# Optimization experiments

Hardware: AMD Instinct MI355X
Metric: run time of the kernel (lower is better)

The kernel has to match this reference:

```python
import jax, jax.numpy as jnp
import numpy as np

N = 10000; E = 320000; NFEAT = 500; NHID = 256; C = 16; K = 64
GAMMA = 4; ALPHA = 0.1; BETA = 1.0; EPS = 0.1; LAMDA = 0.5; W1 = 0.5

def _init(key, shape, scale=0.05):
    return jax.random.normal(key, shape, dtype=jnp.float32) * scale

def setup_inputs():
    key = jax.random.key(0)
    ks = jax.random.split(key, 24)
    return {
        "x": jax.random.normal(ks[0], (N, NFEAT), dtype=jnp.float32),
        "edge_index": jax.random.randint(ks[1], (2, E), 0, N),
        "edge_weight": jax.random.uniform(ks[2], (E,), dtype=jnp.float32),
        "adj_weight": jax.random.uniform(ks[3], (E,), dtype=jnp.float32),
        "connect": jax.random.uniform(ks[4], (N, N), dtype=jnp.float32),
        "confidence_in": jax.random.uniform(ks[5], (2, E), dtype=jnp.float32),
        "lin1_w": _init(ks[6], (NHID, NFEAT)),
        "lin1_b": jnp.zeros((NHID,), jnp.float32),
        "lin2_w": _init(ks[7], (C, NHID)),
        "lin2_b": jnp.zeros((C,), jnp.float32),
        "lin_a_w": _init(ks[8], (NHID, N), 0.01),
        "lin_a_b": jnp.zeros((NHID,), jnp.float32),
        "lin_n_w": _init(ks[9], (C, C)),
        "lin_n_b": jnp.zeros((C,), jnp.float32),
        "left_w": _init(ks[10], (C, C)),
        "att_w": _init(ks[11], (1, C)),
        "v_w": _init(ks[12], (K, NHID)),
        "v_b": jnp.zeros((K,), jnp.float32),
        "W": _init(ks[13], (C, C)),
        "conf_param": jnp.zeros((3,), jnp.float32),
        "b_param": jnp.zeros((1,), jnp.float32),
    }

def _forward(x, edge_index, edge_weight, adj_weight, connect, confidence_in,
             lin1_w, lin1_b, lin2_w, lin2_b, lin_a_w, lin_a_b, lin_n_w, lin_n_b,
             left_w, att_w, v_w, v_b, W, conf_param, b_param):
    row, col = edge_index[0], edge_index[1]

    def spmm(vals, out_idx, M):
        # COO sparse @ dense: scatter-add per-edge vals * gathered rows of M
        return jax.ops.segment_sum(vals[:, None] * M, out_idx, num_segments=N)

    x_a = connect @ lin_a_w.T + lin_a_b            # [N, NHID]
    h = x @ lin1_w.T + lin1_b
    h = jax.nn.relu((1.0 - LAMDA) * h + LAMDA * x_a)
    raw = h                                        # [N, NHID]
    h = h @ lin2_w.T + lin2_b                      # [N, C]

    # neighbor label distribution: row-normalized adj @ one_hot(argmax softmax)
    y_hat = jnp.argmax(jax.nn.softmax(h, axis=1), axis=1)
    one_hot = jax.nn.one_hot(y_hat, C, dtype=h.dtype)
    nei = spmm(adj_weight, row, one_hot[col])
    s = nei.sum(axis=1, keepdims=True)
    nei = jnp.where(s != 0, nei / jnp.where(s == 0, 1.0, s), 0.0)

    x_n = jax.nn.relu(nei @ lin_n_w.T + lin_n_b)
    h = (1.0 - W1) * h + W1 * x_n
    init = h

    # per-edge attention-based confidence mixed with input confidences
    lx = h @ left_w.T
    confi = jax.nn.relu(lx[row] + lx[col])
    confi = jax.nn.sigmoid((confi @ att_w.T)[:, 0])
    w = jax.nn.softmax(conf_param)
    conf = confi * w[0] + confidence_in[0] * w[1] + confidence_in[1] * w[2]  # [E]

    V = raw @ v_w.T + v_b                          # [N, K]
    U = spmm(adj_weight, row, V[col]) @ jnp.linalg.inv(V.T @ V)
    eyeK = jnp.eye(K, dtype=h.dtype)

    def edge_mask_score(score):
        S = score ** 2
        ss = jnp.sort(S)
        q1, q3 = ss[E // 4], ss[3 * E // 4]
        thr = (q3 + 1.5 * (q3 - q1)) * conf        # [E]
        mask = (S < thr).astype(h.dtype)
        return (score + b_param[0]) * mask

    def update_u(U, V):
        SS = edge_mask_score(edge_weight - jnp.sum(U[row] * V[col], axis=1))
        temp = spmm(SS, row, V[col]) + U @ (V.T @ V) + EPS * (h @ (h.T @ V))
        inver = jnp.linalg.inv((1.0 + EPS) * (V.T @ V) + BETA * eyeK)
        return temp @ inver

    def update_v(U, V):
        SS = edge_mask_score(edge_weight - jnp.sum(V[row] * U[col], axis=1))
        # A^T @ U: scatter over col with U[row]
        temp = spmm(SS, col, U[row]) + V @ (U.T @ U) + EPS * (h @ (h.T @ U))
        inver = jnp.linalg.inv((1.0 + EPS) * (U.T @ U) + BETA * eyeK)
        return temp @ inver

    for j in range(GAMMA):
        if j % 2 == 0:
            U = update_u(U, V)
        else:
            V = update_v(U, V)

    prop = U @ (h.T @ V).T                         # [N, C]
    out = (1.0 - ALPHA) * prop + ALPHA * init
    return out @ W

def reference(x, edge_index, edge_weight, adj_weight, connect, confidence_in,
              lin1_w, lin1_b, lin2_w, lin2_b, lin_a_w, lin_a_b, lin_n_w, lin_n_b,
              left_w, att_w, v_w, v_b, W, conf_param, b_param):
    return _forward(x, edge_index, edge_weight, adj_weight, connect, confidence_in,
                    lin1_w, lin1_b, lin2_w, lin2_b, lin_a_w, lin_a_b, lin_n_w, lin_n_b,
                    left_w, att_w, v_w, v_b, W, conf_param, b_param)
```

## Files before the change

kernel.cpp:

```cpp
#include <hip/hip_runtime.h>
#include <cstddef>
#include <cstdint>


constexpr int kN  = 10000;
constexpr int kE  = 320000;
constexpr int kNH = 256;
constexpr int kC  = 16;
constexpr int kK  = 64;

struct SelState {
  int bin1[2]; int rem1[2];
  float thr_base;
};

typedef short bf16x8 __attribute__((ext_vector_type(8)));
typedef float f32x4 __attribute__((ext_vector_type(4)));
typedef ushort ushort8 __attribute__((ext_vector_type(8)));

__device__ __forceinline__ ushort f2bf(float x) {
  unsigned u = __float_as_uint(x);
  unsigned r = (u + 0x7fffu + ((u >> 16) & 1u)) >> 16;
  return (ushort)r;
}
__device__ __forceinline__ float bf2f(ushort h) {
  return __uint_as_float((unsigned)h << 16);
}
__device__ __forceinline__ int swz(int row, int byteInRow) {
  int chunk = (byteInRow >> 4) ^ ((row >> 1) & 3);
  return row * 64 + (chunk << 4) + (byteInRow & 15);
}

__global__ void split_bf(const float* __restrict__ B, ushort* __restrict__ hi,
                         ushort* __restrict__ lo, int N2, int K, int Kp)
{
  int t = blockIdx.x * 256 + threadIdx.x;
  if (t >= N2 * Kp) return;
  int r = t / Kp, c = t % Kp;
  float v = (c < K) ? B[(size_t)r * K + c] : 0.f;
  ushort h = f2bf(v);
  hi[t] = h;
  lo[t] = f2bf(v - bf2f(h));
}

template<int BN, bool ALO>
__global__ __launch_bounds__(256) void gemm_v3(
    const float* __restrict__ A, const ushort* __restrict__ Bhg,
    const ushort* __restrict__ Blg, const float* __restrict__ bias,
    float* __restrict__ out, int M, int K, int Kp, int KR, int outStride)
{
  __shared__ __align__(16) char sAh[64 * 64];
  __shared__ __align__(16) char sAl[ALO ? 64 * 64 : 16];
  __shared__ __align__(16) char sBh[BN * 64];
  __shared__ __align__(16) char sBl[BN * 64];
  const int t = threadIdx.x;
  const int lane = t & 63, w = t >> 6;
  const int bm = blockIdx.x * 64;
  const int k0 = blockIdx.z * KR;
  const int kend = min(K, k0 + KR);
  out += (size_t)blockIdx.z * M * outStride;
  constexpr int WN = BN / 64;
  constexpr int RB = WN;
  const int wc = (w % WN) * 64;
  const int wr = (w / WN) * (RB * 16);
  const int l15 = lane & 15;
  const int lByte = (lane >> 4) * 16;
  const int ar = t >> 2, ac = t & 3;

  f32x4 acc[RB][4] = {};
  for (int kt = k0; kt < kend; kt += 32) {
    {
      int gr = bm + ar, gk = kt + ac * 8;
      float v[8];
      if (gr < M && gk + 8 <= kend) {
        float4 v0 = *reinterpret_cast<const float4*>(A + (size_t)gr * K + gk);
        float4 v1 = *reinterpret_cast<const float4*>(A + (size_t)gr * K + gk + 4);
        v[0] = v0.x; v[1] = v0.y; v[2] = v0.z; v[3] = v0.w;
        v[4] = v1.x; v[5] = v1.y; v[6] = v1.z; v[7] = v1.w;
      } else {
#pragma unroll
        for (int q = 0; q < 8; q++)
          v[q] = (gr < M && gk + q < kend) ? A[(size_t)gr * K + gk + q] : 0.f;
      }
      ushort8 h8, l8;
#pragma unroll
      for (int q = 0; q < 8; q++) {
        ushort h = f2bf(v[q]); h8[q] = h;
        if (ALO) l8[q] = f2bf(v[q] - bf2f(h));
      }
      *reinterpret_cast<ushort8*>(sAh + swz(ar, ac * 16)) = h8;
      if (ALO) *reinterpret_cast<ushort8*>(sAl + swz(ar, ac * 16)) = l8;
    }
#pragma unroll
    for (int i2 = 0; i2 < BN / 64; i2++) {
      int idx = t + i2 * 256;
      int r = idx >> 2, c = idx & 3;
      size_t gb = (size_t)r * Kp + kt + c * 8;
      ushort8 hv = *reinterpret_cast<const ushort8*>(Bhg + gb);
      ushort8 lv = *reinterpret_cast<const ushort8*>(Blg + gb);
      *reinterpret_cast<ushort8*>(sBh + swz(r, c * 16)) = hv;
      *reinterpret_cast<ushort8*>(sBl + swz(r, c * 16)) = lv;
    }
    __syncthreads();
    bf16x8 bh[4], bl[4];
#pragma unroll
    for (int nb = 0; nb < 4; nb++) {
      int rr = wc + nb * 16 + l15;
      bh[nb] = *reinterpret_cast<const bf16x8*>(sBh + swz(rr, lByte));
      bl[nb] = *reinterpret_cast<const bf16x8*>(sBl + swz(rr, lByte));
    }
#pragma unroll
    for (int rb = 0; rb < RB; rb++) {
      int rr = wr + rb * 16 + l15;
      bf16x8 ah = *reinterpret_cast<const bf16x8*>(sAh + swz(rr, lByte));
#pragma unroll
      for (int nb = 0; nb < 4; nb++) {
        acc[rb][nb] = __builtin_amdgcn_mfma_f32_16x16x32_bf16(ah, bh[nb], acc[rb][nb], 0, 0, 0);
        acc[rb][nb] = __builtin_amdgcn_mfma_f32_16x16x32_bf16(ah, bl[nb], acc[rb][nb], 0, 0, 0);
      }
      if (ALO) {
        bf16x8 al = *reinterpret_cast<const bf16x8*>(sAl + swz(rr, lByte));
#pragma unroll
        for (int nb = 0; nb < 4; nb++)
          acc[rb][nb] = __builtin_amdgcn_mfma_f32_16x16x32_bf16(al, bh[nb], acc[rb][nb], 0, 0, 0);
      }
    }
    __syncthreads();
  }
#pragma unroll
  for (int rb = 0; rb < RB; rb++) {
#pragma unroll
    for (int nb = 0; nb < 4; nb++) {
      int colg = wc + nb * 16 + l15;
      float bv = bias ? bias[colg] : 0.f;
#pragma unroll
      for (int j = 0; j < 4; j++) {
        int rowg = bm + wr + rb * 16 + (lane >> 4) * 4 + j;
        if (rowg < M) out[(size_t)rowg * outStride + colg] = acc[rb][nb][j] + bv;
      }
    }
  }
}

__global__ void reduce_raw(const float4* __restrict__ Pa, const float4* px,
                           const float* __restrict__ ba, const float* __restrict__ b1,
                           float4* rawOut)
{
  int t = blockIdx.x * 256 + threadIdx.x;
  if (t >= kN * kNH / 4) return;
  const int sl = kN * kNH / 4;
  float4 s = Pa[t];
#pragma unroll
  for (int p = 1; p < 5; p++) {
    float4 q = Pa[t + (size_t)p * sl];
    s.x += q.x; s.y += q.y; s.z += q.z; s.w += q.w;
  }
  float4 pxv = px[t];
  int c4 = t & 63;
  float4 vba = reinterpret_cast<const float4*>(ba)[c4];
  float4 vb1 = reinterpret_cast<const float4*>(b1)[c4];
  float4 r;
  r.x = fmaxf(0.5f * (s.x + vba.x) + 0.5f * (pxv.x + vb1.x), 0.f);
  r.y = fmaxf(0.5f * (s.y + vba.y) + 0.5f * (pxv.y + vb1.y), 0.f);
  r.z = fmaxf(0.5f * (s.z + vba.z) + 0.5f * (pxv.z + vb1.z), 0.f);
  r.w = fmaxf(0.5f * (s.w + vba.w) + 0.5f * (pxv.w + vb1.w), 0.f);
  rawOut[t] = r;
}

__global__ void gemm_rowdot(const float* __restrict__ A, const float* __restrict__ Bw,
                            const float* __restrict__ bias, float* __restrict__ outm,
                            int M, int N2, int K2)
{
  int t = blockIdx.x * 256 + threadIdx.x;
  if (t >= M * N2) return;
  int i = t / N2, j = t % N2;
  const float4* a = reinterpret_cast<const float4*>(A + (size_t)i * K2);
  const float4* b = reinterpret_cast<const float4*>(Bw + (size_t)j * K2);
  float s = bias ? bias[j] : 0.f;
  int q4 = K2 >> 2;
  for (int q = 0; q < q4; q++) {
    float4 av = a[q], bv = b[q];
    s += av.x * bv.x + av.y * bv.y + av.z * bv.z + av.w * bv.w;
  }
  outm[t] = s;
}

__global__ void argmax16(const float* __restrict__ h, int* __restrict__ y, int n)
{
  int i = blockIdx.x * 256 + threadIdx.x;
  if (i >= n) return;
  const float* r = h + (size_t)i * 16;
  float m = r[0]; int a = 0;
#pragma unroll
  for (int j = 1; j < 16; j++) { float v = r[j]; if (v > m) { m = v; a = j; } }
  y[i] = a;
}

__global__ void scatter_nei(const int* __restrict__ row, const int* __restrict__ col,
                            const float* __restrict__ aw, const int* __restrict__ yhat,
                            float* nei, int E)
{
  int e = blockIdx.x * 256 + threadIdx.x;
  if (e >= E) return;
  atomicAdd(&nei[(size_t)row[e] * 16 + yhat[col[e]]], aw[e]);
}

__global__ void norm_xn_h(const float* __restrict__ nei, const float* __restrict__ h16,
                          const float* __restrict__ lnw, const float* __restrict__ lnb,
                          float* __restrict__ hc, int n)
{
  int i = blockIdx.x * 256 + threadIdx.x;
  if (i >= n) return;
  float nv[16]; float s = 0.f;
#pragma unroll
  for (int c = 0; c < 16; c++) { nv[c] = nei[(size_t)i * 16 + c]; s += nv[c]; }
  float inv = (s != 0.f) ? 1.f / s : 0.f;
#pragma unroll
  for (int j = 0; j < 16; j++) {
    float xn = lnb[j];
#pragma unroll
    for (int c = 0; c < 16; c++) xn += (nv[c] * inv) * lnw[j * 16 + c];
    xn = fmaxf(xn, 0.f);
    hc[(size_t)i * 16 + j] = 0.5f * h16[(size_t)i * 16 + j] + 0.5f * xn;
  }
}

__global__ void edge_conf(const int* __restrict__ row, const int* __restrict__ col,
                          const float* __restrict__ lx, const float* __restrict__ attw,
                          const float* __restrict__ ci, const float* __restrict__ cp,
                          float* __restrict__ conf, int E)
{
  int e = blockIdx.x * 256 + threadIdx.x;
  if (e >= E) return;
  float p0 = cp[0], p1 = cp[1], p2 = cp[2];
  float m = fmaxf(p0, fmaxf(p1, p2));
  float e0 = expf(p0 - m), e1 = expf(p1 - m), e2 = expf(p2 - m);
  float inv = 1.f / (e0 + e1 + e2);
  float w0 = e0 * inv, w1 = e1 * inv, w2 = e2 * inv;
  const float* a = lx + (size_t)row[e] * 16;
  const float* b = lx + (size_t)col[e] * 16;
  float s = 0.f;
#pragma unroll
  for (int c = 0; c < 16; c++) s += fmaxf(a[c] + b[c], 0.f) * attw[c];
  float cf = 1.f / (1.f + expf(-s));
  conf[e] = cf * w0 + ci[e] * w1 + ci[(size_t)E + e] * w2;
}

__global__ void csr_count(const int* __restrict__ row, const int* __restrict__ col,
                          int* cntR, int* cntC, int E)
{
  int e = blockIdx.x * 256 + threadIdx.x;
  if (e >= E) return;
  atomicAdd(&cntR[row[e]], 1);
  atomicAdd(&cntC[col[e]], 1);
}

__global__ __launch_bounds__(1024) void scan2(const int* __restrict__ cntR, const int* __restrict__ cntC,
                                              int* __restrict__ startR, int* __restrict__ startC, int n)
{
  __shared__ int part[1024];
  const int t = threadIdx.x;
  for (int pass = 0; pass < 2; ++pass) {
    const int* cnt = pass ? cntC : cntR;
    int* start = pass ? startC : startR;
    int base = t * 10;
    int loc[10]; int s = 0;
#pragma unroll
    for (int q = 0; q < 10; q++) { int idx = base + q; int v = (idx < n) ? cnt[idx] : 0; loc[q] = v; s += v; }
    part[t] = s;
    __syncthreads();
    for (int off = 1; off < 1024; off <<= 1) {
      int v = part[t];
      int u = (t >= off) ? part[t - off] : 0;
      __syncthreads();
      part[t] = v + u;
      __syncthreads();
    }
    int run = part[t] - s;
#pragma unroll
    for (int q = 0; q < 10; q++) { int idx = base + q; if (idx < n) start[idx] = run; run += loc[q]; }
    if (t == 1023) start[n] = part[1023];
    __syncthreads();
  }
}

__global__ void csr_fill(const int* __restrict__ row, const int* __restrict__ col,
                         const int* __restrict__ startR, const int* __restrict__ startC,
                         int* fillR, int* fillC, int* eR, int* eC,
                         int* othR, int* othC, int E)
{
  int e = blockIdx.x * 256 + threadIdx.x;
  if (e >= E) return;
  int r = row[e], c = col[e];
  int pr = startR[r] + atomicAdd(&fillR[r], 1);
  eR[pr] = e; othR[pr] = c;
  int pc = startC[c] + atomicAdd(&fillC[c], 1);
  eC[pc] = e; othC[pc] = r;
}

__global__ void spmm_gather(const float* __restrict__ vals, const int* __restrict__ start,
                            const int* __restrict__ eids, const int* __restrict__ oth,
                            const float* __restrict__ Msrc, float* __restrict__ T, int n)
{
  int wid = blockIdx.x * 4 + (threadIdx.x >> 6);
  int lane = threadIdx.x & 63;
  if (wid >= n) return;
  int p = start[wid], pend = start[wid + 1];
  float acc = 0.f;
  for (; p + 4 <= pend; p += 4) {
    int e0 = eids[p], e1 = eids[p + 1], e2 = eids[p + 2], e3 = eids[p + 3];
    int o0 = oth[p], o1 = oth[p + 1], o2 = oth[p + 2], o3 = oth[p + 3];
    float m0 = Msrc[(size_t)o0 * 64 + lane];
    float m1 = Msrc[(size_t)o1 * 64 + lane];
    float m2 = Msrc[(size_t)o2 * 64 + lane];
    float m3 = Msrc[(size_t)o3 * 64 + lane];
    acc += vals[e0] * m0 + vals[e1] * m1 + vals[e2] * m2 + vals[e3] * m3;
  }
  for (; p < pend; ++p)
    acc += vals[eids[p]] * Msrc[(size_t)oth[p] * 64 + lane];
  T[(size_t)wid * 64 + lane] = acc;
}

__global__ __launch_bounds__(256) void gram_partial(const float* __restrict__ A, const float* __restrict__ B,
                                                    float* __restrict__ P, int n, int Ka, int chunk)
{
  __shared__ float sA[8 * 64];
  __shared__ float sB[8 * 64];
  const int t = threadIdx.x;
  const int tpa = 256 / Ka;
  const int cpt = 64 / tpa;
  const int a  = t / tpa;
  const int c0 = (t % tpa) * cpt;
  float acc[16];
#pragma unroll
  for (int j = 0; j < 16; j++) acc[j] = 0.f;
  int r0 = blockIdx.x * chunk;
  int r1 = min(n, r0 + chunk);
  for (int rb = r0; rb < r1; rb += 8) {
    int nb = min(8, r1 - rb);
    for (int q = t; q < nb * Ka; q += 256) sA[(q / Ka) * 64 + (q % Ka)] = A[(size_t)(rb + q / Ka) * Ka + (q % Ka)];
    for (int q = t; q < nb * 64; q += 256) sB[q] = B[(size_t)rb * 64 + q];
    __syncthreads();
    for (int r = 0; r < nb; r++) {
      float av = sA[r * 64 + a];
      const float* sb = &sB[r * 64 + c0];
      if (cpt == 16) {
#pragma unroll
        for (int j = 0; j < 16; j++) acc[j] += av * sb[j];
      } else {
#pragma unroll
        for (int j = 0; j < 4; j++) acc[j] += av * sb[j];
      }
    }
    __syncthreads();
  }
  float* p = P + (size_t)blockIdx.x * Ka * 64 + a * 64 + c0;
  if (cpt == 16) {
#pragma unroll
    for (int j = 0; j < 16; j++) p[j] = acc[j];
  } else {
#pragma unroll
    for (int j = 0; j < 4; j++) p[j] = acc[j];
  }
}

__global__ void gram_reduce(const float* __restrict__ P, float* __restrict__ G, int cells, int parts)
{
  int c = blockIdx.x * 256 + threadIdx.x;
  if (c >= cells) return;
  float s = 0.f;
  for (int p = 0; p < parts; p++) s += P[(size_t)p * cells + c];
  G[c] = s;
}

__global__ __launch_bounds__(256) void inverse64_spd(
    const float* __restrict__ G, float* __restrict__ Gi, float alpha, float beta,
    const float* __restrict__ hTX, float* __restrict__ Gp, float* __restrict__ Hp)
{
  __shared__ __align__(16) float A[64 * 132];
  __shared__ __align__(16) float prow[128];
  __shared__ float fcol[64];
  const int t = threadIdx.x;
  for (int q = t; q < 64 * 128; q += 256) {
    int r = q >> 7, c = q & 127;
    float v;
    if (c < 64) v = alpha * G[r * 64 + c] + ((c == r) ? beta : 0.f);
    else        v = (c - 64 == r) ? 1.f : 0.f;
    A[r * 132 + c] = v;
  }
  __syncthreads();
  const int i  = t >> 2;
  const int c0 = (t & 3) * 32;
  for (int k = 0; k < 64; k++) {
    if (t < 128) prow[t] = A[k * 132 + t];
    else if (t < 192) fcol[t - 128] = A[(t - 128) * 132 + k];
    __syncthreads();
    float pinv = 1.f / prow[k];
    float f = fcol[i];
    float4* Ar = reinterpret_cast<float4*>(&A[i * 132 + c0]);
    const float4* pr = reinterpret_cast<const float4*>(&prow[c0]);
    if (i == k) {
#pragma unroll
      for (int j = 0; j < 8; j++) {
        float4 p = pr[j];
        p.x *= pinv; p.y *= pinv; p.z *= pinv; p.w *= pinv;
        Ar[j] = p;
      }
    } else {
#pragma unroll
      for (int j = 0; j < 8; j++) {
        float4 p = pr[j]; float4 av = Ar[j];
        av.x -= f * (p.x * pinv); av.y -= f * (p.y * pinv);
        av.z -= f * (p.z * pinv); av.w -= f * (p.w * pinv);
        Ar[j] = av;
      }
    }
    __syncthreads();
  }
  for (int q = t; q < 4096; q += 256) Gi[q] = A[(q >> 6) * 132 + 64 + (q & 63)];
  if (Gp) {
    for (int q = t; q < 4096; q += 256) {
      int r = q >> 6, k = q & 63;
      float s = 0.f;
#pragma unroll 8
      for (int j = 0; j < 64; j++) s += G[r * 64 + j] * A[j * 132 + 64 + k];
      Gp[q] = s;
    }
    for (int q = t; q < 1024; q += 256) {
      int c = q >> 6, k = q & 63;
      float s = 0.f;
#pragma unroll 8
      for (int j = 0; j < 64; j++) s += hTX[c * 64 + j] * A[j * 132 + 64 + k];
      Hp[q] = 0.1f * s;
    }
  }
}

__global__ void edge_score(const float* __restrict__ ew, const int* __restrict__ row,
                           const int* __restrict__ col, const float* __restrict__ Ma,
                           const float* __restrict__ Mb, float* __restrict__ score,
                           int* __restrict__ hist1, int* __restrict__ h2a,
                           int* __restrict__ h2b, int E)
{
  int e = blockIdx.x * 256 + threadIdx.x;
  if (e < 65536) { hist1[e] = 0; h2a[e] = 0; h2b[e] = 0; }
  if (e >= E) return;
  const float4* a = reinterpret_cast<const float4*>(Ma + (size_t)row[e] * 64);
  const float4* b = reinterpret_cast<const float4*>(Mb + (size_t)col[e] * 64);
  float s = 0.f;
#pragma unroll
  for (int q = 0; q < 16; q++) {
    float4 av = a[q], bv = b[q];
    s += av.x * bv.x + av.y * bv.y + av.z * bv.z + av.w * bv.w;
  }
  score[e] = ew[e] - s;
}

__global__ void hist_pass1(const float* __restrict__ score, int* __restrict__ h, int E)
{
  int e = blockIdx.x * 256 + threadIdx.x;
  if (e >= E) return;
  float sc = score[e];
  unsigned u = __float_as_uint(sc * sc);
  atomicAdd(&h[u >> 16], 1);
}

__global__ void hist_pass2(const float* __restrict__ score, const SelState* __restrict__ sel,
                           int* __restrict__ h2a, int* __restrict__ h2b, int E)
{
  int e = blockIdx.x * 256 + threadIdx.x;
  if (e >= E) return;
  float sc = score[e];
  unsigned u = __float_as_uint(sc * sc);
  int top = (int)(u >> 16);
  if (top == sel->bin1[0]) atomicAdd(&h2a[u & 0xFFFF], 1);
  if (top == sel->bin1[1]) atomicAdd(&h2b[u & 0xFFFF], 1);
}

__global__ __launch_bounds__(256) void select_scan(
    const int* __restrict__ h0, const int* __restrict__ h1,
    int stage, SelState* sel)
{
  const int t = threadIdx.x;
  __shared__ int part[256];
  __shared__ int foundBin[2];
  __shared__ float qsh[2];
  const int per = 65536 / 256;
  for (int tgt = 0; tgt < 2; tgt++) {
    const int* H = tgt ? h1 : h0;
    int R = (stage == 1) ? (tgt ? (3 * kE / 4) : (kE / 4)) : sel->rem1[tgt];
    int lsum = 0;
    for (int b = 0; b < per; b++) lsum += H[t * per + b];
    part[t] = lsum;
    __syncthreads();
    for (int off = 1; off < 256; off <<= 1) {
      int v = part[t];
      int u = (t >= off) ? part[t - off] : 0;
      __syncthreads();
      part[t] = v + u;
      __syncthreads();
    }
    int cum = part[t] - lsum;
    int fb = -1, fr = 0;
    for (int b = 0; b < per; b++) {
      int c = H[t * per + b];
      if (R >= cum && R < cum + c) { fb = t * per + b; fr = R - cum; }
      cum += c;
    }
    if (fb >= 0) {
      foundBin[tgt] = fb;
      if (stage == 1) { sel->bin1[tgt] = fb; sel->rem1[tgt] = fr; }
    }
    __syncthreads();
    if (stage == 2 && t == 0) {
      unsigned u = ((unsigned)sel->bin1[tgt] << 16) | (unsigned)foundBin[tgt];
      qsh[tgt] = __uint_as_float(u);
    }
    __syncthreads();
  }
  if (stage == 2 && t == 0) {
    float q1 = qsh[0], q3 = qsh[1];
    sel->thr_base = q3 + 1.5f * (q3 - q1);
  }
}

__global__ void mask_SS(const float* __restrict__ score, const float* __restrict__ conf,
                        const SelState* __restrict__ sel, const float* __restrict__ bp,
                        float* __restrict__ SS, int E)
{
  int e = blockIdx.x * 256 + threadIdx.x;
  if (e >= E) return;
  float sc = score[e];
  float thr = sel->thr_base * conf[e];
  SS[e] = (sc * sc < thr) ? (sc + bp[0]) : 0.f;
}

__global__ void out_fused(const float* __restrict__ T, const float* __restrict__ Gi,
                          const float* __restrict__ X, const float* __restrict__ Gp,
                          const float* __restrict__ hc, const float* __restrict__ Hp,
                          float* __restrict__ Out, int n)
{
  int t = blockIdx.x * 256 + threadIdx.x;
  if (t >= n * 64) return;
  int i = t >> 6, k = t & 63;
  const float* ti = T + (size_t)i * 64;
  float s = 0.f;
#pragma unroll 8
  for (int j = 0; j < 64; j++) s += ti[j] * Gi[j * 64 + k];
  if (X) {
    const float* xi = X + (size_t)i * 64;
    float s2 = 0.f;
#pragma unroll 8
    for (int j = 0; j < 64; j++) s2 += xi[j] * Gp[j * 64 + k];
    s += s2;
    float s3 = 0.f;
#pragma unroll
    for (int c = 0; c < 16; c++) s3 += hc[(size_t)i * 16 + c] * Hp[c * 64 + k];
    s += s3;
  }
  Out[t] = s;
}

__global__ __launch_bounds__(256) void final_out(
    const float* __restrict__ Um, const float* __restrict__ hTV,
    const float* __restrict__ hc, const float* __restrict__ Wm,
    float* __restrict__ out, int n)
{
  __shared__ float sh[1024];
  __shared__ float sW[256];
  for (int q = threadIdx.x; q < 1024; q += 256) sh[q] = hTV[q];
  sW[threadIdx.x] = Wm[threadIdx.x & 255];
  __syncthreads();
  int i = blockIdx.x * 256 + threadIdx.x;
  if (i >= n) return;
  const float* u = Um + (size_t)i * 64;
  float pre[16];
#pragma unroll
  for (int c = 0; c < 16; c++) {
    float s = 0.f;
#pragma unroll
    for (int k = 0; k < 64; k++) s += u[k] * sh[c * 64 + k];
    pre[c] = 0.9f * s + 0.1f * hc[(size_t)i * 16 + c];
  }
#pragma unroll
  for (int j = 0; j < 16; j++) {
    float o = 0.f;
#pragma unroll
    for (int c = 0; c < 16; c++) o += pre[c] * sW[c * 16 + j];
    out[(size_t)i * 16 + j] = o;
  }
}

extern "C" void kernel_launch(void* const* d_in, const int* in_sizes, int n_in,
                              void* d_out, int out_size, void* d_ws, size_t ws_size,
                              hipStream_t stream)
{
  const float* x       = (const float*)d_in[0];
  const int*   eidx    = (const int*)d_in[1];
  const float* ew      = (const float*)d_in[2];
  const float* aw      = (const float*)d_in[3];
  const float* connect = (const float*)d_in[4];
  const float* ci      = (const float*)d_in[5];
  const float* lin1_w  = (const float*)d_in[6];
  const float* lin1_b  = (const float*)d_in[7];
  const float* lin2_w  = (const float*)d_in[8];
  const float* lin2_b  = (const float*)d_in[9];
  const float* lin_a_w = (const float*)d_in[10];
  const float* lin_a_b = (const float*)d_in[11];
  const float* lin_n_w = (const float*)d_in[12];
  const float* lin_n_b = (const float*)d_in[13];
  const float* left_w  = (const float*)d_in[14];
  const float* att_w   = (const float*)d_in[15];
  const float* v_w     = (const float*)d_in[16];
  const float* v_b     = (const float*)d_in[17];
  const float* Wm      = (const float*)d_in[18];
  const float* conf_p  = (const float*)d_in[19];
  const float* b_param = (const float*)d_in[20];
  const int* row = eidx;
  const int* col = eidx + kE;
  float* out = (float*)d_out;

  char* base = (char*)d_ws;
  size_t off = 0;
  auto alloc = [&](size_t bytes) -> void* {
    void* p = base + off;
    off += bytes;
    off = (off + 255) & ~(size_t)255;
    return p;
  };
  float* raw   = (float*)alloc((size_t)kN * kNH * 4);
  float* h16   = (float*)alloc((size_t)kN * kC * 4);
  float* hC    = (float*)alloc((size_t)kN * kC * 4);
  float* nei   = (float*)alloc((size_t)kN * kC * 4);
  float* lx    = (float*)alloc((size_t)kN * kC * 4);
  int*   yhat  = (int*)alloc((size_t)kN * 4);
  float* conf  = (float*)alloc((size_t)kE * 4);
  float* Va    = (float*)alloc((size_t)kN * kK * 4);
  float* Vb    = (float*)alloc((size_t)kN * kK * 4);
  float* Ua    = (float*)alloc((size_t)kN * kK * 4);
  float* Ub    = (float*)alloc((size_t)kN * kK * 4);
  float* T     = (float*)alloc((size_t)kN * kK * 4);
  float* score = (float*)alloc((size_t)kE * 4);
  float* SS    = (float*)alloc((size_t)kE * 4);
  float* G     = (float*)alloc(64 * 64 * 4);
  float* Gi    = (float*)alloc(64 * 64 * 4);
  float* Gp    = (float*)alloc(64 * 64 * 4);
  float* hTX   = (float*)alloc(kC * kK * 4);
  float* Hp    = (float*)alloc(kC * kK * 4);
  int* hist1   = (int*)alloc(65536 * 4);
  int* h2a     = (int*)alloc(65536 * 4);
  int* h2b     = (int*)alloc(65536 * 4);
  SelState* sel = (SelState*)alloc(sizeof(SelState));
  int* cntR    = (int*)alloc((size_t)kN * 4);
  int* cntC    = (int*)alloc((size_t)kN * 4);
  int* fillR   = (int*)alloc((size_t)kN * 4);
  int* fillC   = (int*)alloc((size_t)kN * 4);
  int* startR  = (int*)alloc((size_t)(kN + 1) * 4);
  int* startC  = (int*)alloc((size_t)(kN + 1) * 4);
  int* eR      = (int*)alloc((size_t)kE * 4);
  int* eC      = (int*)alloc((size_t)kE * 4);
  int* othR    = (int*)alloc((size_t)kE * 4);
  int* othC    = (int*)alloc((size_t)kE * 4);
  float* P     = (float*)alloc((size_t)100 * 4096 * 4);
  const int KpC = 10016, KpX = 512, KpV = 256;
  ushort* BcH = (ushort*)alloc((size_t)256 * KpC * 2);
  ushort* BcL = (ushort*)alloc((size_t)256 * KpC * 2);
  ushort* BxH = (ushort*)alloc((size_t)256 * KpX * 2);
  ushort* BxL = (ushort*)alloc((size_t)256 * KpX * 2);
  ushort* BvH = (ushort*)alloc((size_t)64 * KpV * 2);
  ushort* BvL = (ushort*)alloc((size_t)64 * KpV * 2);
  float* Pbig  = (float*)alloc((size_t)5 * kN * kNH * 4);

  const int eg  = (kE + 255) / 256;
  const int nkg = (kN * kK + 255) / 256;
  const int gwg = (kN + 3) / 4;

  split_bf<<<(256 * KpC + 255) / 256, 256, 0, stream>>>(lin_a_w, BcH, BcL, 256, 10000, KpC);
  split_bf<<<(256 * KpX + 255) / 256, 256, 0, stream>>>(lin1_w, BxH, BxL, 256, 500, KpX);
  split_bf<<<(64 * KpV + 255) / 256, 256, 0, stream>>>(v_w, BvH, BvL, 64, 256, KpV);

  {
    size_t csrSpan = (size_t)((char*)(fillC + kN) - (char*)cntR);
    (void)hipMemsetAsync(cntR, 0, csrSpan, stream);
  }
  csr_count<<<eg, 256, 0, stream>>>(row, col, cntR, cntC, kE);
  scan2<<<1, 1024, 0, stream>>>(cntR, cntC, startR, startC, kN);
  csr_fill<<<eg, 256, 0, stream>>>(row, col, startR, startC, fillR, fillC, eR, eC, othR, othC, kE);

  gemm_v3<256, false><<<dim3(157, 1, 5), 256, 0, stream>>>(
      connect, BcH, BcL, nullptr, Pbig, kN, 10000, KpC, 2016, kNH);
  gemm_v3<256, true><<<dim3(157, 1, 1), 256, 0, stream>>>(
      x, BxH, BxL, nullptr, raw, kN, 500, KpX, 512, kNH);
  reduce_raw<<<(kN * kNH / 4 + 255) / 256, 256, 0, stream>>>(
      (const float4*)Pbig, (const float4*)raw, lin_a_b, lin1_b, (float4*)raw);
  gemm_rowdot<<<(kN * kC + 255) / 256, 256, 0, stream>>>(raw, lin2_w, lin2_b, h16, kN, kC, kNH);
  argmax16<<<(kN + 255) / 256, 256, 0, stream>>>(h16, yhat, kN);
  (void)hipMemsetAsync(nei, 0, (size_t)kN * kC * 4, stream);
  scatter_nei<<<eg, 256, 0, stream>>>(row, col, aw, yhat, nei, kE);
  norm_xn_h<<<(kN + 255) / 256, 256, 0, stream>>>(nei, h16, lin_n_w, lin_n_b, hC, kN);
  gemm_rowdot<<<(kN * kC + 255) / 256, 256, 0, stream>>>(hC, left_w, nullptr, lx, kN, kC, kC);
  edge_conf<<<eg, 256, 0, stream>>>(row, col, lx, att_w, ci, conf_p, conf, kE);
  gemm_v3<64, true><<<dim3(157, 1, 1), 256, 0, stream>>>(
      raw, BvH, BvL, v_b, Va, kN, 256, KpV, 256, kK);

  float* Ucur = Ua; float* Unxt = Ub;
  float* Vcur = Va; float* Vnxt = Vb;

  gram_partial<<<100, 256, 0, stream>>>(Vcur, Vcur, P, kN, 64, 100);
  gram_reduce<<<16, 256, 0, stream>>>(P, G, 4096, 100);
  inverse64_spd<<<1, 256, 0, stream>>>(G, Gi, 1.0f, 0.0f, nullptr, nullptr, nullptr);
  spmm_gather<<<gwg, 256, 0, stream>>>(aw, startR, eR, othR, Vcur, T, kN);
  out_fused<<<nkg, 256, 0, stream>>>(T, Gi, nullptr, nullptr, nullptr, nullptr, Ucur, kN);

  for (int j = 0; j < 4; j++) {
    bool upd_u = ((j & 1) == 0);
    const float* Ma = upd_u ? Ucur : Vcur;
    const float* Mb = upd_u ? Vcur : Ucur;
    edge_score<<<eg, 256, 0, stream>>>(ew, row, col, Ma, Mb, score, hist1, h2a, h2b, kE);
    hist_pass1<<<eg, 256, 0, stream>>>(score, hist1, kE);
    select_scan<<<1, 256, 0, stream>>>(hist1, hist1, 1, sel);
    hist_pass2<<<eg, 256, 0, stream>>>(score, sel, h2a, h2b, kE);
    select_scan<<<1, 256, 0, stream>>>(h2a, h2b, 2, sel);
    mask_SS<<<eg, 256, 0, stream>>>(score, conf, sel, b_param, SS, kE);

    const float* Xcur = upd_u ? Ucur : Vcur;
    const float* Moth = upd_u ? Vcur : Ucur;
    float* Xout = upd_u ? Unxt : Vnxt;
    gram_partial<<<100, 256, 0, stream>>>(Moth, Moth, P, kN, 64, 100);
    gram_reduce<<<16, 256, 0, stream>>>(P, G, 4096, 100);
    gram_partial<<<100, 256, 0, stream>>>(hC, Moth, P, kN, 16, 100);
    gram_reduce<<<4, 256, 0, stream>>>(P, hTX, 1024, 100);
    inverse64_spd<<<1, 256, 0, stream>>>(G, Gi, 1.1f, 1.0f, hTX, Gp, Hp);
    if (upd_u) spmm_gather<<<gwg, 256, 0, stream>>>(SS, startR, eR, othR, Vcur, T, kN);
    else       spmm_gather<<<gwg, 256, 0, stream>>>(SS, startC, eC, othC, Ucur, T, kN);
    out_fused<<<nkg, 256, 0, stream>>>(T, Gi, Xcur, Gp, hC, Hp, Xout, kN);
    if (upd_u) { float* tmp = Ucur; Ucur = Unxt; Unxt = tmp; }
    else       { float* tmp = Vcur; Vcur = Vnxt; Vnxt = tmp; }
  }

  gram_partial<<<100, 256, 0, stream>>>(hC, Vcur, P, kN, 16, 100);
  gram_reduce<<<4, 256, 0, stream>>>(P, hTX, 1024, 100);
  final_out<<<(kN + 255) / 256, 256, 0, stream>>>(Ucur, hTX, hC, Wm, out, kN);
}
```

Baseline: 2.529 ms.

## Fuse many small kernels across the GNN pipeline and retune split-K

The change merges several launches into fewer kernels. The two gram passes become one gram2 kernel. Histogram building moves into edge_score, and histogram zeroing moves into out_fused. Mask computation now happens inline in spmm_gather. The lin2 projection and argmax are fused, with argmax done by a shuffle reduction. select_scan now runs on 1024 threads with vector loads, out_fused is vectorised to float4, and the connect GEMM split-K goes from 5 to 6 slices. The aim is to cut launch overhead and intermediate memory traffic, at the cost of recomputing the mask per gathered edge and some extra branching.

Result: faster. 2.220 ms (-12.2%).

```diff
diff --git a/kernel.cpp b/kernel.cpp
--- a/kernel.cpp
+++ b/kernel.cpp
@@ -151,7 +151,7 @@
   const int sl = kN * kNH / 4;
   float4 s = Pa[t];
 #pragma unroll
-  for (int p = 1; p < 5; p++) {
+  for (int p = 1; p < 6; p++) {
     float4 q = Pa[t + (size_t)p * sl];
     s.x += q.x; s.y += q.y; s.z += q.z; s.w += q.w;
   }
@@ -167,6 +167,61 @@
   rawOut[t] = r;
 }
 
+__global__ void h16_argmax(const float* __restrict__ raw, const float* __restrict__ w2,
+                           const float* __restrict__ b2, float* __restrict__ h16,
+                           int* __restrict__ yhat, int n)
+{
+  int t = blockIdx.x * 256 + threadIdx.x;
+  if (t >= n * 16) return;
+  int i = t >> 4, j = t & 15;
+  const float4* a = reinterpret_cast<const float4*>(raw + (size_t)i * 256);
+  const float4* b = reinterpret_cast<const float4*>(w2 + (size_t)j * 256);
+  float s = b2[j];
+#pragma unroll 8
+  for (int q = 0; q < 64; q++) {
+    float4 av = a[q], bv = b[q];
+    s += av.x * bv.x + av.y * bv.y + av.z * bv.z + av.w * bv.w;
+  }
+  h16[t] = s;
+  float m = s; int am = j;
+#pragma unroll
+  for (int off = 1; off < 16; off <<= 1) {
+    float om = __shfl_xor(m, off);
+    int oa = __shfl_xor(am, off);
+    if (om > m || (om == m && oa < am)) { m = om; am = oa; }
+  }
+  if (j == 0) yhat[i] = am;
+}
+
+__global__ void scatter_nei(const int* __restrict__ row, const int* __restrict__ col,
+                            const float* __restrict__ aw, const int* __restrict__ yhat,
+                            float* nei, int E)
+{
+  int e = blockIdx.x * 256 + threadIdx.x;
+  if (e >= E) return;
+  atomicAdd(&nei[(size_t)row[e] * 16 + yhat[col[e]]], aw[e]);
+}
+
+__global__ void norm_xn_h(const float* __restrict__ nei, const float* __restrict__ h16,
+                          const float* __restrict__ lnw, const float* __restrict__ lnb,
+                          float* __restrict__ hc, int n)
+{
+  int i = blockIdx.x * 256 + threadIdx.x;
+  if (i >= n) return;
+  float nv[16]; float s = 0.f;
+#pragma unroll
+  for (int c = 0; c < 16; c++) { nv[c] = nei[(size_t)i * 16 + c]; s += nv[c]; }
+  float inv = (s != 0.f) ? 1.f / s : 0.f;
+#pragma unroll
+  for (int j = 0; j < 16; j++) {
+    float xn = lnb[j];
+#pragma unroll
+    for (int c = 0; c < 16; c++) xn += (nv[c] * inv) * lnw[j * 16 + c];
+    xn = fmaxf(xn, 0.f);
+    hc[(size_t)i * 16 + j] = 0.5f * h16[(size_t)i * 16 + j] + 0.5f * xn;
+  }
+}
+
 __global__ void gemm_rowdot(const float* __restrict__ A, const float* __restrict__ Bw,
                             const float* __restrict__ bias, float* __restrict__ outm,
                             int M, int N2, int K2)
@@ -185,46 +240,6 @@
   outm[t] = s;
 }
 
-__global__ void argmax16(const float* __restrict__ h, int* __restrict__ y, int n)
-{
-  int i = blockIdx.x * 256 + threadIdx.x;
-  if (i >= n) return;
-  const float* r = h + (size_t)i * 16;
-  float m = r[0]; int a = 0;
-#pragma unroll
-  for (int j = 1; j < 16; j++) { float v = r[j]; if (v > m) { m = v; a = j; } }
-  y[i] = a;
-}
-
-__global__ void scatter_nei(const int* __restrict__ row, const int* __restrict__ col,
-                            const float* __restrict__ aw, const int* __restrict__ yhat,
-                            float* nei, int E)
-{
-  int e = blockIdx.x * 256 + threadIdx.x;
-  if (e >= E) return;
-  atomicAdd(&nei[(size_t)row[e] * 16 + yhat[col[e]]], aw[e]);
-}
-
-__global__ void norm_xn_h(const float* __restrict__ nei, const float* __restrict__ h16,
-                          const float* __restrict__ lnw, const float* __restrict__ lnb,
-                          float* __restrict__ hc, int n)
-{
-  int i = blockIdx.x * 256 + threadIdx.x;
-  if (i >= n) return;
-  float nv[16]; float s = 0.f;
-#pragma unroll
-  for (int c = 0; c < 16; c++) { nv[c] = nei[(size_t)i * 16 + c]; s += nv[c]; }
-  float inv = (s != 0.f) ? 1.f / s : 0.f;
-#pragma unroll
-  for (int j = 0; j < 16; j++) {
-    float xn = lnb[j];
-#pragma unroll
-    for (int c = 0; c < 16; c++) xn += (nv[c] * inv) * lnw[j * 16 + c];
-    xn = fmaxf(xn, 0.f);
-    hc[(size_t)i * 16 + j] = 0.5f * h16[(size_t)i * 16 + j] + 0.5f * xn;
-  }
-}
-
 __global__ void edge_conf(const int* __restrict__ row, const int* __restrict__ col,
                           const float* __restrict__ lx, const float* __restrict__ attw,
                           const float* __restrict__ ci, const float* __restrict__ cp,
@@ -298,13 +313,22 @@
   eC[pc] = e; othC[pc] = r;
 }
 
-__global__ void spmm_gather(const float* __restrict__ vals, const int* __restrict__ start,
+__global__ void spmm_gather(const float* __restrict__ vals, const float* __restrict__ score,
+                            const float* __restrict__ conf, const SelState* __restrict__ sel,
+                            const float* __restrict__ bp, const int* __restrict__ start,
                             const int* __restrict__ eids, const int* __restrict__ oth,
                             const float* __restrict__ Msrc, float* __restrict__ T, int n)
 {
   int wid = blockIdx.x * 4 + (threadIdx.x >> 6);
   int lane = threadIdx.x & 63;
   if (wid >= n) return;
+  float tb = 0.f, bp0 = 0.f;
+  if (!vals) { tb = sel->thr_base; bp0 = bp[0]; }
+  auto val = [&](int e) -> float {
+    if (vals) return vals[e];
+    float sc = score[e];
+    return (sc * sc < tb * conf[e]) ? (sc + bp0) : 0.f;
+  };
   int p = start[wid], pend = start[wid + 1];
   float acc = 0.f;
   for (; p + 4 <= pend; p += 4) {
@@ -314,63 +338,64 @@
     float m1 = Msrc[(size_t)o1 * 64 + lane];
     float m2 = Msrc[(size_t)o2 * 64 + lane];
     float m3 = Msrc[(size_t)o3 * 64 + lane];
-    acc += vals[e0] * m0 + vals[e1] * m1 + vals[e2] * m2 + vals[e3] * m3;
+    acc += val(e0) * m0 + val(e1) * m1 + val(e2) * m2 + val(e3) * m3;
   }
   for (; p < pend; ++p)
-    acc += vals[eids[p]] * Msrc[(size_t)oth[p] * 64 + lane];
+    acc += val(eids[p]) * Msrc[(size_t)oth[p] * 64 + lane];
   T[(size_t)wid * 64 + lane] = acc;
 }
 
-__global__ __launch_bounds__(256) void gram_partial(const float* __restrict__ A, const float* __restrict__ B,
-                                                    float* __restrict__ P, int n, int Ka, int chunk)
-{
-  __shared__ float sA[8 * 64];
-  __shared__ float sB[8 * 64];
+__global__ __launch_bounds__(256) void gram2_partial(
+    const float* __restrict__ Moth, const float* __restrict__ hc,
+    float* __restrict__ P, int n, int chunk)
+{
+  __shared__ float sM[8 * 64];
+  __shared__ float sH[8 * 16];
   const int t = threadIdx.x;
-  const int tpa = 256 / Ka;
-  const int cpt = 64 / tpa;
-  const int a  = t / tpa;
-  const int c0 = (t % tpa) * cpt;
-  float acc[16];
-#pragma unroll
-  for (int j = 0; j < 16; j++) acc[j] = 0.f;
+  const int aG = t >> 2, cG0 = (t & 3) * 16;
+  const int aH = t >> 4, cH0 = (t & 15) * 4;
+  float accG[16];
+  float accH[4];
+#pragma unroll
+  for (int j = 0; j < 16; j++) accG[j] = 0.f;
+#pragma unroll
+  for (int j = 0; j < 4; j++) accH[j] = 0.f;
   int r0 = blockIdx.x * chunk;
   int r1 = min(n, r0 + chunk);
   for (int rb = r0; rb < r1; rb += 8) {
     int nb = min(8, r1 - rb);
-    for (int q = t; q < nb * Ka; q += 256) sA[(q / Ka) * 64 + (q % Ka)] = A[(size_t)(rb + q / Ka) * Ka + (q % Ka)];
-    for (int q = t; q < nb * 64; q += 256) sB[q] = B[(size_t)rb * 64 + q];
+    for (int q = t; q < nb * 64; q += 256) sM[q] = Moth[(size_t)rb * 64 + q];
+    for (int q = t; q < nb * 16; q += 256) sH[q] = hc[(size_t)rb * 16 + q];
     __syncthreads();
     for (int r = 0; r < nb; r++) {
-      float av = sA[r * 64 + a];
-      const float* sb = &sB[r * 64 + c0];
-      if (cpt == 16) {
-#pragma unroll
-        for (int j = 0; j < 16; j++) acc[j] += av * sb[j];
-      } else {
-#pragma unroll
-        for (int j = 0; j < 4; j++) acc[j] += av * sb[j];
-      }
-    }
-    __syncthreads();
-  }
-  float* p = P + (size_t)blockIdx.x * Ka * 64 + a * 64 + c0;
-  if (cpt == 16) {
-#pragma unroll
-    for (int j = 0; j < 16; j++) p[j] = acc[j];
-  } else {
-#pragma unroll
-    for (int j = 0; j < 4; j++) p[j] = acc[j];
-  }
-}
-
-__global__ void gram_reduce(const float* __restrict__ P, float* __restrict__ G, int cells, int parts)
+      float avG = sM[r * 64 + aG];
+      const float* sbG = &sM[r * 64 + cG0];
+#pragma unroll
+      for (int j = 0; j < 16; j++) accG[j] += avG * sbG[j];
+      float avH = sH[r * 16 + aH];
+      const float* sbH = &sM[r * 64 + cH0];
+#pragma unroll
+      for (int j = 0; j < 4; j++) accH[j] += avH * sbH[j];
+    }
+    __syncthreads();
+  }
+  float* p1 = P + (size_t)blockIdx.x * 5120 + aG * 64 + cG0;
+#pragma unroll
+  for (int j = 0; j < 16; j++) p1[j] = accG[j];
+  float* p2 = P + (size_t)blockIdx.x * 5120 + 4096 + aH * 64 + cH0;
+#pragma unroll
+  for (int j = 0; j < 4; j++) p2[j] = accH[j];
+}
+
+__global__ void gram_reduce2(const float* __restrict__ P, float* __restrict__ G,
+                             float* __restrict__ hTX, int parts)
 {
   int c = blockIdx.x * 256 + threadIdx.x;
-  if (c >= cells) return;
+  if (c >= 5120) return;
   float s = 0.f;
-  for (int p = 0; p < parts; p++) s += P[(size_t)p * cells + c];
-  G[c] = s;
+  for (int p = 0; p < parts; p++) s += P[(size_t)p * 5120 + c];
+  if (c < 4096) G[c] = s;
+  else hTX[c - 4096] = s;
 }
 
 __global__ __launch_bounds__(256) void inverse64_spd(
@@ -439,11 +464,9 @@
 __global__ void edge_score(const float* __restrict__ ew, const int* __restrict__ row,
                            const int* __restrict__ col, const float* __restrict__ Ma,
                            const float* __restrict__ Mb, float* __restrict__ score,
-                           int* __restrict__ hist1, int* __restrict__ h2a,
-                           int* __restrict__ h2b, int E)
+                           int* __restrict__ hist1, int E)
 {
   int e = blockIdx.x * 256 + threadIdx.x;
-  if (e < 65536) { hist1[e] = 0; h2a[e] = 0; h2b[e] = 0; }
   if (e >= E) return;
   const float4* a = reinterpret_cast<const float4*>(Ma + (size_t)row[e] * 64);
   const float4* b = reinterpret_cast<const float4*>(Mb + (size_t)col[e] * 64);
@@ -453,16 +476,10 @@
     float4 av = a[q], bv = b[q];
     s += av.x * bv.x + av.y * bv.y + av.z * bv.z + av.w * bv.w;
   }
-  score[e] = ew[e] - s;
-}
-
-__global__ void hist_pass1(const float* __restrict__ score, int* __restrict__ h, int E)
-{
-  int e = blockIdx.x * 256 + threadIdx.x;
-  if (e >= E) return;
-  float sc = score[e];
+  float sc = ew[e] - s;
+  score[e] = sc;
   unsigned u = __float_as_uint(sc * sc);
-  atomicAdd(&h[u >> 16], 1);
+  atomicAdd(&hist1[u >> 16], 1);
 }
 
 __global__ void hist_pass2(const float* __restrict__ score, const SelState* __restrict__ sel,
@@ -477,23 +494,28 @@
   if (top == sel->bin1[1]) atomicAdd(&h2b[u & 0xFFFF], 1);
 }
 
-__global__ __launch_bounds__(256) void select_scan(
+__global__ __launch_bounds__(1024) void select_scan(
     const int* __restrict__ h0, const int* __restrict__ h1,
     int stage, SelState* sel)
 {
   const int t = threadIdx.x;
-  __shared__ int part[256];
+  __shared__ int part[1024];
   __shared__ int foundBin[2];
   __shared__ float qsh[2];
-  const int per = 65536 / 256;
+  const int per = 64;
   for (int tgt = 0; tgt < 2; tgt++) {
     const int* H = tgt ? h1 : h0;
+    const int4* H4 = reinterpret_cast<const int4*>(H + t * per);
     int R = (stage == 1) ? (tgt ? (3 * kE / 4) : (kE / 4)) : sel->rem1[tgt];
     int lsum = 0;
-    for (int b = 0; b < per; b++) lsum += H[t * per + b];
+#pragma unroll
+    for (int b = 0; b < 16; b++) {
+      int4 v = H4[b];
+      lsum += v.x + v.y + v.z + v.w;
+    }
     part[t] = lsum;
     __syncthreads();
-    for (int off = 1; off < 256; off <<= 1) {
+    for (int off = 1; off < 1024; off <<= 1) {
       int v = part[t];
       int u = (t >= off) ? part[t - off] : 0;
       __syncthreads();
@@ -502,10 +524,19 @@
     }
     int cum = part[t] - lsum;
     int fb = -1, fr = 0;
-    for (int b = 0; b < per; b++) {
-      int c = H[t * per + b];
-      if (R >= cum && R < cum + c) { fb = t * per + b; fr = R - cum; }
-      cum += c;
+#pragma unroll
+    for (int b = 0; b < 16; b++) {
+      int4 v = H4[b];
+      int c0 = v.x, c1 = v.y, c2 = v.z, c3 = v.w;
+      int bb = t * per + b * 4;
+      if (R >= cum && R < cum + c0) { fb = bb; fr = R - cum; }
+      cum += c0;
+      if (fb < 0 && R >= cum && R < cum + c1) { fb = bb + 1; fr = R - cum; }
+      cum += c1;
+      if (fb < 0 && R >= cum && R < cum + c2) { fb = bb + 2; fr = R - cum; }
+      cum += c2;
+      if (fb < 0 && R >= cum && R < cum + c3) { fb = bb + 3; fr = R - cum; }
+      cum += c3;
     }
     if (fb >= 0) {
       foundBin[tgt] = fb;
@@ -524,41 +555,48 @@
   }
 }
 
-__global__ void mask_SS(const float* __restrict__ score, const float* __restrict__ conf,
-                        const SelState* __restrict__ sel, const float* __restrict__ bp,
-                        float* __restrict__ SS, int E)
-{
-  int e = blockIdx.x * 256 + threadIdx.x;
-  if (e >= E) return;
-  float sc = score[e];
-  float thr = sel->thr_base * conf[e];
-  SS[e] = (sc * sc < thr) ? (sc + bp[0]) : 0.f;
-}
-
 __global__ void out_fused(const float* __restrict__ T, const float* __restrict__ Gi,
                           const float* __restrict__ X, const float* __restrict__ Gp,
                           const float* __restrict__ hc, const float* __restrict__ Hp,
-                          float* __restrict__ Out, int n)
+                          float* __restrict__ Out, int n,
+                          int* __restrict__ hist1, int* __restrict__ h2a,
+                          int* __restrict__ h2b)
 {
   int t = blockIdx.x * 256 + threadIdx.x;
-  if (t >= n * 64) return;
-  int i = t >> 6, k = t & 63;
+  if (t < 65536) { hist1[t] = 0; h2a[t] = 0; h2b[t] = 0; }
+  if (t >= n * 16) return;
+  int i = t >> 4, kq = t & 15;
   const float* ti = T + (size_t)i * 64;
-  float s = 0.f;
+  const float4* G4 = reinterpret_cast<const float4*>(Gi);
+  float4 s = make_float4(0.f, 0.f, 0.f, 0.f);
 #pragma unroll 8
-  for (int j = 0; j < 64; j++) s += ti[j] * Gi[j * 64 + k];
+  for (int j = 0; j < 64; j++) {
+    float tv = ti[j];
+    float4 g = G4[j * 16 + kq];
+    s.x += tv * g.x; s.y += tv * g.y; s.z += tv * g.z; s.w += tv * g.w;
+  }
   if (X) {
     const float* xi = X + (size_t)i * 64;
-    float s2 = 0.f;
+    const float4* Gp4 = reinterpret_cast<const float4*>(Gp);
+    float4 s2 = make_float4(0.f, 0.f, 0.f, 0.f);
 #pragma unroll 8
-    for (int j = 0; j < 64; j++) s2 += xi[j] * Gp[j * 64 + k];
-    s += s2;
-    float s3 = 0.f;
-#pragma unroll
-    for (int c = 0; c < 16; c++) s3 += hc[(size_t)i * 16 + c] * Hp[c * 64 + k];
-    s += s3;
-  }
-  Out[t] = s;
+    for (int j = 0; j < 64; j++) {
+      float xv = xi[j];
+      float4 g = Gp4[j * 16 + kq];
+      s2.x += xv * g.x; s2.y += xv * g.y; s2.z += xv * g.z; s2.w += xv * g.w;
+    }
+    s.x += s2.x; s.y += s2.y; s.z += s2.z; s.w += s2.w;
+    const float4* Hp4 = reinterpret_cast<const float4*>(Hp);
+    float4 s3 = make_float4(0.f, 0.f, 0.f, 0.f);
+#pragma unroll
+    for (int c = 0; c < 16; c++) {
+      float hv = hc[(size_t)i * 16 + c];
+      float4 g = Hp4[c * 16 + kq];
+      s3.x += hv * g.x; s3.y += hv * g.y; s3.z += hv * g.z; s3.w += hv * g.w;
+    }
+    s.x += s3.x; s.y += s3.y; s.z += s3.z; s.w += s3.w;
+  }
+  *reinterpret_cast<float4*>(Out + (size_t)i * 64 + kq * 4) = s;
 }
 
 __global__ __launch_bounds__(256) void final_out(
@@ -641,7 +679,6 @@
   float* Ub    = (float*)alloc((size_t)kN * kK * 4);
   float* T     = (float*)alloc((size_t)kN * kK * 4);
   float* score = (float*)alloc((size_t)kE * 4);
-  float* SS    = (float*)alloc((size_t)kE * 4);
   float* G     = (float*)alloc(64 * 64 * 4);
   float* Gi    = (float*)alloc(64 * 64 * 4);
   float* Gp    = (float*)alloc(64 * 64 * 4);
@@ -661,7 +698,7 @@
   int* eC      = (int*)alloc((size_t)kE * 4);
   int* othR    = (int*)alloc((size_t)kE * 4);
   int* othC    = (int*)alloc((size_t)kE * 4);
-  float* P     = (float*)alloc((size_t)100 * 4096 * 4);
+  float* P     = (float*)alloc((size_t)100 * 5120 * 4);
   const int KpC = 10016, KpX = 512, KpV = 256;
   ushort* BcH = (ushort*)alloc((size_t)256 * KpC * 2);
   ushort* BcL = (ushort*)alloc((size_t)256 * KpC * 2);
@@ -669,10 +706,10 @@
   ushort* BxL = (ushort*)alloc((size_t)256 * KpX * 2);
   ushort* BvH = (ushort*)alloc((size_t)64 * KpV * 2);
   ushort* BvL = (ushort*)alloc((size_t)64 * KpV * 2);
-  float* Pbig  = (float*)alloc((size_t)5 * kN * kNH * 4);
+  float* Pbig  = (float*)alloc((size_t)6 * kN * kNH * 4);
 
   const int eg  = (kE + 255) / 256;
-  const int nkg = (kN * kK + 255) / 256;
+  const int ofg = (kN * 16 + 255) / 256;
   const int gwg = (kN + 3) / 4;
 
   split_bf<<<(256 * KpC + 255) / 256, 256, 0, stream>>>(lin_a_w, BcH, BcL, 256, 10000, KpC);
@@ -687,14 +724,13 @@
   scan2<<<1, 1024, 0, stream>>>(cntR, cntC, startR, startC, kN);
   csr_fill<<<eg, 256, 0, stream>>>(row, col, startR, startC, fillR, fillC, eR, eC, othR, othC, kE);
 
-  gemm_v3<256, false><<<dim3(157, 1, 5), 256, 0, stream>>>(
-      connect, BcH, BcL, nullptr, Pbig, kN, 10000, KpC, 2016, kNH);
+  gemm_v3<256, false><<<dim3(157, 1, 6), 256, 0, stream>>>(
+      connect, BcH, BcL, nullptr, Pbig, kN, 10000, KpC, 1696, kNH);
   gemm_v3<256, true><<<dim3(157, 1, 1), 256, 0, stream>>>(
       x, BxH, BxL, nullptr, raw, kN, 500, KpX, 512, kNH);
   reduce_raw<<<(kN * kNH / 4 + 255) / 256, 256, 0, stream>>>(
       (const float4*)Pbig, (const float4*)raw, lin_a_b, lin1_b, (float4*)raw);
-  gemm_rowdot<<<(kN * kC + 255) / 256, 256, 0, stream>>>(raw, lin2_w, lin2_b, h16, kN, kC, kNH);
-  argmax16<<<(kN + 255) / 256, 256, 0, stream>>>(h16, yhat, kN);
+  h16_argmax<<<(kN * 16 + 255) / 256, 256, 0, stream>>>(raw, lin2_w, lin2_b, h16, yhat, kN);
   (void)hipMemsetAsync(nei, 0, (size_t)kN * kC * 4, stream);
   scatter_nei<<<eg, 256, 0, stream>>>(row, col, aw, yhat, nei, kE);
   norm_xn_h<<<(kN + 255) / 256, 256, 0, stream>>>(nei, h16, lin_n_w, lin_n_b, hC, kN);
@@ -706,39 +742,39 @@
   float* Ucur = Ua; float* Unxt = Ub;
   float* Vcur = Va; float* Vnxt = Vb;
 
-  gram_partial<<<100, 256, 0, stream>>>(Vcur, Vcur, P, kN, 64, 100);
-  gram_reduce<<<16, 256, 0, stream>>>(P, G, 4096, 100);
+  gram2_partial<<<100, 256, 0, stream>>>(Vcur, hC, P, kN, 100);
+  gram_reduce2<<<20, 256, 0, stream>>>(P, G, hTX, 100);
   inverse64_spd<<<1, 256, 0, stream>>>(G, Gi, 1.0f, 0.0f, nullptr, nullptr, nullptr);
-  spmm_gather<<<gwg, 256, 0, stream>>>(aw, startR, eR, othR, Vcur, T, kN);
-  out_fused<<<nkg, 256, 0, stream>>>(T, Gi, nullptr, nullptr, nullptr, nullptr, Ucur, kN);
+  spmm_gather<<<gwg, 256, 0, stream>>>(aw, nullptr, nullptr, nullptr, nullptr,
+                                       startR, eR, othR, Vcur, T, kN);
+  out_fused<<<ofg, 256, 0, stream>>>(T, Gi, nullptr, nullptr, nullptr, nullptr,
+                                     Ucur, kN, hist1, h2a, h2b);
 
   for (int j = 0; j < 4; j++) {
     bool upd_u = ((j & 1) == 0);
     const float* Ma = upd_u ? Ucur : Vcur;
     const float* Mb = upd_u ? Vcur : Ucur;
-    edge_score<<<eg, 256, 0, stream>>>(ew, row, col, Ma, Mb, score, hist1, h2a, h2b, kE);
-    hist_pass1<<<eg, 256, 0, stream>>>(score, hist1, kE);
-    select_scan<<<1, 256, 0, stream>>>(hist1, hist1, 1, sel);
+    edge_score<<<eg, 256, 0, stream>>>(ew, row, col, Ma, Mb, score, hist1, kE);
+    select_scan<<<1, 1024, 0, stream>>>(hist1, hist1, 1, sel);
     hist_pass2<<<eg, 256, 0, stream>>>(score, sel, h2a, h2b, kE);
-    select_scan<<<1, 256, 0, stream>>>(h2a, h2b, 2, sel);
-    mask_SS<<<eg, 256, 0, stream>>>(score, conf, sel, b_param, SS, kE);
+    select_scan<<<1, 1024, 0, stream>>>(h2a, h2b, 2, sel);
 
     const float* Xcur = upd_u ? Ucur : Vcur;
     const float* Moth = upd_u ? Vcur : Ucur;
     float* Xout = upd_u ? Unxt : Vnxt;
-    gram_partial<<<100, 256, 0, stream>>>(Moth, Moth, P, kN, 64, 100);
-    gram_reduce<<<16, 256, 0, stream>>>(P, G, 4096, 100);
-    gram_partial<<<100, 256, 0, stream>>>(hC, Moth, P, kN, 16, 100);
-    gram_reduce<<<4, 256, 0, stream>>>(P, hTX, 1024, 100);
+    gram2_partial<<<100, 256, 0, stream>>>(Moth, hC, P, kN, 100);
+    gram_reduce2<<<20, 256, 0, stream>>>(P, G, hTX, 100);
     inverse64_spd<<<1, 256, 0, stream>>>(G, Gi, 1.1f, 1.0f, hTX, Gp, Hp);
-    if (upd_u) spmm_gather<<<gwg, 256, 0, stream>>>(SS, startR, eR, othR, Vcur, T, kN);
-    else       spmm_gather<<<gwg, 256, 0, stream>>>(SS, startC, eC, othC, Ucur, T, kN);
-    out_fused<<<nkg, 256, 0, stream>>>(T, Gi, Xcur, Gp, hC, Hp, Xout, kN);
+    if (upd_u) spmm_gather<<<gwg, 256, 0, stream>>>(nullptr, score, conf, sel, b_param,
+                                                    startR, eR, othR, Vcur, T, kN);
+    else       spmm_gather<<<gwg, 256, 0, stream>>>(nullptr, score, conf, sel, b_param,
+                                                    startC, eC, othC, Ucur, T, kN);
+    out_fused<<<ofg, 256, 0, stream>>>(T, Gi, Xcur, Gp, hC, Hp, Xout, kN, hist1, h2a, h2b);
     if (upd_u) { float* tmp = Ucur; Ucur = Unxt; Unxt = tmp; }
     else       { float* tmp = Vcur; Vcur = Vnxt; Vnxt = tmp; }
   }
 
-  gram_partial<<<100, 256, 0, stream>>>(hC, Vcur, P, kN, 16, 100);
-  gram_reduce<<<4, 256, 0, stream>>>(P, hTX, 1024, 100);
+  gram2_partial<<<100, 256, 0, stream>>>(Vcur, hC, P, kN, 100);
+  gram_reduce2<<<20, 256, 0, stream>>>(P, G, hTX, 100);
   final_out<<<(kN + 255) / 256, 256, 0, stream>>>(Ucur, hTX, hC, Wm, out, kN);
 }
```
